# Kernel tuning notes

Measured on AMD Instinct MI355X. Metric: run time of the kernel, lower is better.

The kernel has to match this reference:

```python
import jax, jax.numpy as jnp
import numpy as np

D = 2048  # filter_dim
B = 4096  # tokens per TTT step


def setup_inputs() -> dict:
    key = jax.random.key(0)
    ks = jax.random.split(key, 8)
    s = 1.0 / np.sqrt(D)  # kaiming-ish scale so activations stay O(1)
    return {
        "src": jax.random.normal(ks[0], (B, D), jnp.float32),
        "theta_k": jax.random.normal(ks[1], (D, D), jnp.float32) * s,
        "theta_q": jax.random.normal(ks[2], (D, D), jnp.float32) * s,
        "theta_v": jax.random.normal(ks[3], (D, D), jnp.float32) * s,
        "W": jax.random.normal(ks[4], (D, D), jnp.float32) * s,
        "b": jnp.zeros((D,), jnp.float32),
        "lr_w": jax.random.uniform(ks[5], (D, D), jnp.float32) * 0.1,
        "lr_b": jax.random.uniform(ks[6], (D,), jnp.float32) * 0.1,
    }


def reference(src, theta_k, theta_q, theta_v, W, b, lr_w, lr_b):
    # Projections: src is [B, D], thetas are [D, D]
    train_view = src @ theta_k           # [B, D]
    label_view = src @ theta_v           # [B, D]
    test_view = src @ theta_q            # [B, D]

    target = label_view - train_view     # reconstruction target
    pred = train_view @ W.T + b          # nn.Linear(train_view)
    err = pred - target                  # [B, D]

    # Analytic grads of MSELoss (mean over B*D elements) wrt W ([D,D]) and b ([D])
    n = err.size  # B * D (static)
    coef = 2.0 / n
    gW = coef * (err.T @ train_view)     # [D, D], matches w.weight layout
    gb = coef * jnp.sum(err, axis=0)     # [D]

    # Per-element learning-rate SGD step (the in-place parameter rewrite)
    W_new = W - lr_w * gW
    b_new = b - lr_b * gb

    # Query with updated weights + residual
    z = test_view @ W_new.T + b_new + test_view
    return z
```

## Files before the change

kernel.cpp:

```cpp
#include <hip/hip_runtime.h>
#include <hip/hip_bf16.h>
#include <hip/hip_fp8.h>
#include <stdint.h>

#define D_DIM 2048
#define B_TOK 4096
#define COEF (2.0f / 8388608.0f)

typedef __bf16 bf16x8 __attribute__((ext_vector_type(8)));
typedef float  f32x4  __attribute__((ext_vector_type(4)));
typedef int    i32x8  __attribute__((ext_vector_type(8)));

__device__ __forceinline__ unsigned short f2bf(float f) {
  return __builtin_bit_cast(unsigned short, (__bf16)f);
}
__device__ __forceinline__ float bf2f(unsigned short u) {
  return (float)__builtin_bit_cast(__bf16, u);
}
__device__ __forceinline__ unsigned char f2f8(float f) {
  __hip_fp8_e4m3 v(f);
  return v.__x;
}

__device__ __forceinline__ void async16(const void* g, void* l) {
  __builtin_amdgcn_global_load_lds(
      (__attribute__((address_space(1))) void*)(g),
      (__attribute__((address_space(3))) void*)(l),
      16, 0, 0);
}

__device__ __forceinline__ void gemm_core_256(const unsigned short* __restrict__ Ablk,
                                              const unsigned short* __restrict__ Bblk,
                                              const int lda, const int ldb, const int KC,
                                              unsigned short* As, unsigned short* Bs,
                                              f32x4 acc[4][4]) {
  const int tid  = threadIdx.x;
  const int lane = tid & 63;
  const int wv   = tid >> 6;
  const int wm   = wv >> 1;
  const int wn   = wv & 1;
  const int t    = lane & 15;
  const int quad = lane >> 4;
  const int lrow = lane >> 3;
  const int kq   = lane & 7;
  const int kqs  = kq ^ lrow;

  const int nk = KC >> 6;

  auto stageA2 = [&](int buf, int kt, int l0) {
    const int k0 = kt << 6;
    unsigned short* Ad = As + buf * 16384;
#pragma unroll
    for (int l = l0; l < l0 + 2; ++l) {
      const int seg = wv * 4 + l;
      const int r   = seg * 8 + lrow;
      async16(Ablk + (size_t)r * lda + k0 + kqs * 8, Ad + seg * 512);
    }
  };
  auto stageB1 = [&](int buf, int kt, int l) {
    const int k0 = kt << 6;
    unsigned short* Bd = Bs + buf * 8192;
    const int seg = wv * 2 + l;
    const int r   = seg * 8 + lrow;
    async16(Bblk + (size_t)r * ldb + k0 + kqs * 8, Bd + seg * 512);
  };

  stageA2(0, 0, 0); stageA2(0, 0, 2); stageB1(0, 0, 0); stageB1(0, 0, 1);
  if (nk > 1) { stageA2(1, 1, 0); stageA2(1, 1, 2); stageB1(1, 1, 0); stageB1(1, 1, 1); }
  if (nk > 1) asm volatile("s_waitcnt vmcnt(6)" ::: "memory");
  else        asm volatile("s_waitcnt vmcnt(0)" ::: "memory");
  __builtin_amdgcn_s_barrier();

  int cur = 0;
  for (int kt = 0; kt < nk; ++kt) {
    const unsigned short* Ac = As + cur * 16384;
    const unsigned short* Bc = Bs + cur * 8192;
    const int nb = (cur >= 1) ? cur - 1 : 2;
    const bool pf = (kt + 2 < nk);

    bf16x8 af[4], bfr[4];
#pragma unroll
    for (int i = 0; i < 4; ++i) {
      const int rm = wm * 64 + i * 16 + t;
      af[i]  = *(const bf16x8*)(Ac + rm * 64 + ((quad) ^ (rm & 7)) * 8);
      const int rn = wn * 64 + i * 16 + t;
      bfr[i] = *(const bf16x8*)(Bc + rn * 64 + ((quad) ^ (rn & 7)) * 8);
    }
    __builtin_amdgcn_sched_barrier(0);
    if (pf) { stageA2(nb, kt + 2, 0); stageB1(nb, kt + 2, 0); }
    __builtin_amdgcn_sched_barrier(0);
    __builtin_amdgcn_s_barrier();
    asm volatile("s_waitcnt lgkmcnt(0)" ::: "memory");
    __builtin_amdgcn_sched_barrier(0);
    __builtin_amdgcn_s_setprio(1);
#pragma unroll
    for (int i = 0; i < 4; ++i)
#pragma unroll
      for (int j = 0; j < 4; ++j)
        acc[i][j] = __builtin_amdgcn_mfma_f32_16x16x32_bf16(af[i], bfr[j], acc[i][j], 0, 0, 0);
    __builtin_amdgcn_s_setprio(0);
    __builtin_amdgcn_sched_barrier(0);
    __builtin_amdgcn_s_barrier();

#pragma unroll
    for (int i = 0; i < 4; ++i) {
      const int rm = wm * 64 + i * 16 + t;
      af[i]  = *(const bf16x8*)(Ac + rm * 64 + ((4 + quad) ^ (rm & 7)) * 8);
      const int rn = wn * 64 + i * 16 + t;
      bfr[i] = *(const bf16x8*)(Bc + rn * 64 + ((4 + quad) ^ (rn & 7)) * 8);
    }
    __builtin_amdgcn_sched_barrier(0);
    if (pf) { stageA2(nb, kt + 2, 2); stageB1(nb, kt + 2, 1); }
    __builtin_amdgcn_sched_barrier(0);
    if (pf)               asm volatile("s_waitcnt vmcnt(6)" ::: "memory");
    else if (kt + 1 < nk) asm volatile("s_waitcnt vmcnt(0)" ::: "memory");
    __builtin_amdgcn_s_barrier();
    asm volatile("s_waitcnt lgkmcnt(0)" ::: "memory");
    __builtin_amdgcn_sched_barrier(0);
    __builtin_amdgcn_s_setprio(1);
#pragma unroll
    for (int i = 0; i < 4; ++i)
#pragma unroll
      for (int j = 0; j < 4; ++j)
        acc[i][j] = __builtin_amdgcn_mfma_f32_16x16x32_bf16(af[i], bfr[j], acc[i][j], 0, 0, 0);
    __builtin_amdgcn_s_setprio(0);
    __builtin_amdgcn_sched_barrier(0);
    __builtin_amdgcn_s_barrier();

    cur = (cur == 2) ? 0 : cur + 1;
  }
}

#define GEMM_PROLOGUE256(AP, BP, LDAv, LDBv, KCv)                              \
  __shared__ __align__(16) unsigned short As[3 * 16384];                       \
  __shared__ __align__(16) unsigned short Bs[3 * 8192];                        \
  const int lin = blockIdx.y * 16 + blockIdx.x;                                \
  const int swz = (lin & 7) * 32 + (lin >> 3);                                 \
  const int bx = swz & 15, by = swz >> 4;                                      \
  const unsigned short* Ablk = (AP) + (size_t)by * 256 * (LDAv);               \
  const unsigned short* Bblk = (BP) + (size_t)bx * 128 * (LDBv);               \
  f32x4 acc[4][4];                                                             \
  _Pragma("unroll") for (int i = 0; i < 4; ++i)                                \
  _Pragma("unroll") for (int j = 0; j < 4; ++j)                                \
      acc[i][j] = (f32x4){0.f, 0.f, 0.f, 0.f};                                 \
  gemm_core_256(Ablk, Bblk, (LDAv), (LDBv), (KCv), As, Bs, acc);               \
  const int lane = threadIdx.x & 63;                                           \
  const int wv = threadIdx.x >> 6;                                             \
  const int wm = wv >> 1, wn = wv & 1;                                         \
  const int t = lane & 15, quad = lane >> 4;                                   \
  const int gm_base = by * 256 + wm * 64;                                      \
  const int gn_base = bx * 128 + wn * 64;

__device__ __forceinline__ void gemm_core_f8(const unsigned char* __restrict__ Ablk,
                                             const unsigned char* __restrict__ Bblk,
                                             const int lda, const int ldb, const int KC,
                                             unsigned char* As, unsigned char* Bs,
                                             f32x4 acc[4][4]) {
  const int tid  = threadIdx.x;
  const int lane = tid & 63;
  const int wv   = tid >> 6;
  const int wm   = wv & 1, wn = wv >> 1;
  const int t    = lane & 15;
  const int quad = lane >> 4;
  const int lrow = lane >> 3;
  const int kq   = lane & 7;
  const int kqs  = kq ^ lrow;

  const int nk = KC >> 7;
  for (int kt = 0; kt < nk; ++kt) {
    const int k0 = kt << 7;
#pragma unroll
    for (int l = 0; l < 4; ++l) {
      const int seg = wv * 4 + l;
      const int r   = seg * 8 + lrow;
      async16(Ablk + (size_t)r * lda + k0 + kqs * 16, As + seg * 1024);
      async16(Bblk + (size_t)r * ldb + k0 + kqs * 16, Bs + seg * 1024);
    }
    __syncthreads();
    i32x8 af[4];
#pragma unroll
    for (int i = 0; i < 4; ++i) {
      const int rm = wm * 64 + i * 16 + t;
      const unsigned char* base = As + rm * 128;
      const int x = rm & 7;
      const uint4 lo = *(const uint4*)(base + (((quad << 1)    ) ^ x) * 16);
      const uint4 hi = *(const uint4*)(base + (((quad << 1) | 1) ^ x) * 16);
      af[i] = (i32x8){(int)lo.x, (int)lo.y, (int)lo.z, (int)lo.w,
                      (int)hi.x, (int)hi.y, (int)hi.z, (int)hi.w};
    }
#pragma unroll
    for (int j = 0; j < 4; ++j) {
      const int rn = wn * 64 + j * 16 + t;
      const unsigned char* base = Bs + rn * 128;
      const int x = rn & 7;
      const uint4 lo = *(const uint4*)(base + (((quad << 1)    ) ^ x) * 16);
      const uint4 hi = *(const uint4*)(base + (((quad << 1) | 1) ^ x) * 16);
      const i32x8 bq = (i32x8){(int)lo.x, (int)lo.y, (int)lo.z, (int)lo.w,
                               (int)hi.x, (int)hi.y, (int)hi.z, (int)hi.w};
#pragma unroll
      for (int i = 0; i < 4; ++i)
        acc[i][j] = __builtin_amdgcn_mfma_scale_f32_16x16x128_f8f6f4(
            af[i], bq, acc[i][j], 0, 0, 0, 127, 0, 127);
    }
    __syncthreads();
  }
}

#define GEMM8_PROLOGUE(AP, BP, LDAv, LDBv, KCv)                                \
  __shared__ __align__(16) unsigned char As8[128 * 128];                       \
  __shared__ __align__(16) unsigned char Bs8[128 * 128];                       \
  const unsigned char* Ablk = (AP) + (size_t)blockIdx.y * 128 * (LDAv);        \
  const unsigned char* Bblk = (BP) + (size_t)blockIdx.x * 128 * (LDBv);        \
  f32x4 acc[4][4];                                                             \
  _Pragma("unroll") for (int i = 0; i < 4; ++i)                                \
  _Pragma("unroll") for (int j = 0; j < 4; ++j)                                \
      acc[i][j] = (f32x4){0.f, 0.f, 0.f, 0.f};                                 \
  gemm_core_f8(Ablk, Bblk, (LDAv), (LDBv), (KCv), As8, Bs8, acc);              \
  const int lane = threadIdx.x & 63;                                           \
  const int wv = threadIdx.x >> 6;                                             \
  const int wm = wv & 1, wn = wv >> 1;                                         \
  const int t = lane & 15, quad = lane >> 4;                                   \
  const int gm_base = blockIdx.y * 128 + wm * 64;                              \
  const int gn_base = blockIdx.x * 128 + wn * 64;

__global__ __launch_bounds__(256) void gemm_train_f8(
    const unsigned char* __restrict__ srcA,
    const unsigned char* __restrict__ thkT8,
    unsigned char* __restrict__ src_cat_f8,
    unsigned char* __restrict__ trainT8) {
  GEMM8_PROLOGUE(srcA, thkT8, 4096, 2048, 2048)
  unsigned char* scr = ((wv >> 1) ? Bs8 : As8) + (wv & 1) * 2304;
#pragma unroll
  for (int p = 0; p < 2; ++p) {
#pragma unroll
    for (int jl = 0; jl < 2; ++jl) {
      const int j = p * 2 + jl;
      const int gn = gn_base + j * 16 + t;
#pragma unroll
      for (int i = 0; i < 4; ++i) {
        const int gm0 = gm_base + i * 16 + quad * 4;
        uchar4 pk = make_uchar4(f2f8(acc[i][j][0]), f2f8(acc[i][j][1]),
                                f2f8(acc[i][j][2]), f2f8(acc[i][j][3]));
        src_cat_f8[(size_t)(gm0 + 0) * 4096 + gn] = pk.x;
        src_cat_f8[(size_t)(gm0 + 1) * 4096 + gn] = pk.y;
        src_cat_f8[(size_t)(gm0 + 2) * 4096 + gn] = pk.z;
        src_cat_f8[(size_t)(gm0 + 3) * 4096 + gn] = pk.w;
        *(uchar4*)(scr + (jl * 16 + t) * 72 + i * 16 + quad * 4) = pk;
      }
    }
    __syncthreads();
    const int row = lane >> 3, chunk = lane & 7;
#pragma unroll
    for (int q = 0; q < 4; ++q) {
      const int rr = q * 8 + row;
      const uint2 v = *(const uint2*)(scr + rr * 72 + chunk * 8);
      *(uint2*)(trainT8 + (size_t)(gn_base + p * 32 + rr) * B_TOK + gm_base + chunk * 8) = v;
    }
    __syncthreads();
  }
}

__global__ __launch_bounds__(512, 2) void gemm_test(
    const unsigned short* __restrict__ src_bf,
    const unsigned short* __restrict__ thqT,
    unsigned short* __restrict__ testv) {
  GEMM_PROLOGUE256(src_bf, thqT, 2048, 2048, 2048)
#pragma unroll
  for (int i = 0; i < 4; ++i) {
#pragma unroll
    for (int j = 0; j < 4; ++j) {
      const int gm0 = gm_base + i * 16 + quad * 4;
      const int gn  = gn_base + j * 16 + t;
#pragma unroll
      for (int r = 0; r < 4; ++r)
        testv[(size_t)(gm0 + r) * D_DIM + gn] = f2bf(acc[i][j][r]);
    }
  }
}

__global__ __launch_bounds__(256) void gemm_err_f8(
    const unsigned char* __restrict__ src_cat_f8,
    const unsigned char* __restrict__ Wcat_f8,
    const float* __restrict__ bvec,
    unsigned char* __restrict__ errT8,
    float* __restrict__ gb) {
  GEMM8_PROLOGUE(src_cat_f8, Wcat_f8, 4096, 4096, 4096)
  unsigned char* scr = ((wv >> 1) ? Bs8 : As8) + (wv & 1) * 2304;
#pragma unroll
  for (int p = 0; p < 2; ++p) {
#pragma unroll
    for (int jl = 0; jl < 2; ++jl) {
      const int j = p * 2 + jl;
      const int gn = gn_base + j * 16 + t;
      const float bias = bvec[gn];
      float cs = 0.f;
#pragma unroll
      for (int i = 0; i < 4; ++i) {
        const float e0 = acc[i][j][0] + bias, e1 = acc[i][j][1] + bias;
        const float e2 = acc[i][j][2] + bias, e3 = acc[i][j][3] + bias;
        *(uchar4*)(scr + (jl * 16 + t) * 72 + i * 16 + quad * 4) =
            make_uchar4(f2f8(e0), f2f8(e1), f2f8(e2), f2f8(e3));
        cs += e0 + e1 + e2 + e3;
      }
      cs += __shfl_xor(cs, 16);
      cs += __shfl_xor(cs, 32);
      if (quad == 0) atomicAdd(&gb[gn], cs);
    }
    __syncthreads();
    const int row = lane >> 3, chunk = lane & 7;
#pragma unroll
    for (int q = 0; q < 4; ++q) {
      const int rr = q * 8 + row;
      const uint2 v = *(const uint2*)(scr + rr * 72 + chunk * 8);
      *(uint2*)(errT8 + (size_t)(gn_base + p * 32 + rr) * B_TOK + gm_base + chunk * 8) = v;
    }
    __syncthreads();
  }
}

__global__ __launch_bounds__(256) void gemm_gw_f8(
    const unsigned char* __restrict__ errT8,
    const unsigned char* __restrict__ trainT8,
    float* __restrict__ P0, float* __restrict__ P1) {
  const int z = blockIdx.z;
  const unsigned char* Abase = errT8 + z * 2048;
  const unsigned char* Bbase = trainT8 + z * 2048;
  GEMM8_PROLOGUE(Abase, Bbase, B_TOK, B_TOK, 2048)
  float* P = (z == 0) ? P0 : P1;
#pragma unroll
  for (int i = 0; i < 4; ++i) {
#pragma unroll
    for (int j = 0; j < 4; ++j) {
      const int gm0 = gm_base + i * 16 + quad * 4;
      const int gn  = gn_base + j * 16 + t;
#pragma unroll
      for (int r = 0; r < 4; ++r)
        P[(size_t)(gm0 + r) * D_DIM + gn] = acc[i][j][r];
    }
  }
}

__global__ __launch_bounds__(256) void wnew_reduce(
    const float* __restrict__ P0, const float* __restrict__ P1,
    const float* __restrict__ W, const float* __restrict__ lr_w,
    unsigned short* __restrict__ Wnew) {
  const int i = blockIdx.x * 256 + threadIdx.x;
  const float4 p0 = ((const float4*)P0)[i];
  const float4 p1 = ((const float4*)P1)[i];
  const float4 w  = ((const float4*)W)[i];
  const float4 l  = ((const float4*)lr_w)[i];
  ((ushort4*)Wnew)[i] = make_ushort4(
      f2bf(w.x - l.x * (COEF * (p0.x + p1.x))),
      f2bf(w.y - l.y * (COEF * (p0.y + p1.y))),
      f2bf(w.z - l.z * (COEF * (p0.z + p1.z))),
      f2bf(w.w - l.w * (COEF * (p0.w + p1.w))));
}

__global__ __launch_bounds__(512, 2) void gemm_out(
    const unsigned short* __restrict__ testv,
    const unsigned short* __restrict__ Wnew,
    const float* __restrict__ bvec,
    const float* __restrict__ lr_b,
    const float* __restrict__ gb,
    float* __restrict__ out) {
  GEMM_PROLOGUE256(testv, Wnew, 2048, 2048, 2048)
#pragma unroll
  for (int j = 0; j < 4; ++j) {
    const int gn = gn_base + j * 16 + t;
    const float bias = bvec[gn] - lr_b[gn] * (COEF * gb[gn]);
#pragma unroll
    for (int i = 0; i < 4; ++i) {
      const int gm0 = gm_base + i * 16 + quad * 4;
#pragma unroll
      for (int r = 0; r < 4; ++r) {
        const size_t idx = (size_t)(gm0 + r) * D_DIM + gn;
        out[idx] = acc[i][j][r] + bias + bf2f(testv[idx]);
      }
    }
  }
}

__global__ __launch_bounds__(256) void cvt_all(const float* __restrict__ src,
                                               const float* __restrict__ W,
                                               unsigned short* __restrict__ src_bf,
                                               unsigned char* __restrict__ src_cat_f8,
                                               unsigned char* __restrict__ Wcat_f8,
                                               float* __restrict__ gb) {
  const int i = blockIdx.x * 256 + threadIdx.x;
  if (i < 512) ((float4*)gb)[i] = (float4){0.f, 0.f, 0.f, 0.f};
  if (i < 2097152) {
    const int m = i >> 9, c = i & 511;
    const float4 v = ((const float4*)src)[i];
    ((ushort4*)src_bf)[i] = make_ushort4(f2bf(v.x), f2bf(v.y), f2bf(v.z), f2bf(v.w));
    *(uchar4*)(src_cat_f8 + (size_t)m * 4096 + 2048 + c * 4) =
        make_uchar4(f2f8(v.x), f2f8(v.y), f2f8(v.z), f2f8(v.w));
  } else {
    const int j = i - 2097152;
    const int n = j >> 9, c = j & 511;
    const float4 v = ((const float4*)W)[j];
    *(uchar4*)(Wcat_f8 + (size_t)n * 4096 + c * 4) =
        make_uchar4(f2f8(v.x), f2f8(v.y), f2f8(v.z), f2f8(v.w));
  }
}

__global__ __launch_bounds__(256) void tcvt(
    const float* __restrict__ thk, const float* __restrict__ thq,
    const float* __restrict__ thv,
    unsigned char* __restrict__ thkT8, unsigned short* __restrict__ thqT,
    unsigned char* __restrict__ Wcat_f8) {
  __shared__ float tile[32][33];
  const int z = blockIdx.z;
  const int bx = blockIdx.x * 32, by = blockIdx.y * 32;
  const int tx = threadIdx.x & 31, ty = threadIdx.x >> 5;
#pragma unroll
  for (int l = 0; l < 4; ++l) {
    const int r = ty + l * 8;
    const size_t idx = (size_t)(by + r) * D_DIM + bx + tx;
    tile[r][tx] = (z == 0) ? thk[idx] : (z == 1) ? thq[idx] : (thk[idx] - thv[idx]);
  }
  __syncthreads();
#pragma unroll
  for (int l = 0; l < 4; ++l) {
    const int r = ty + l * 8;
    if (z == 0)
      thkT8[(size_t)(bx + r) * 2048 + by + tx] = f2f8(tile[tx][r]);
    else if (z == 1)
      thqT[(size_t)(bx + r) * 2048 + by + tx] = f2bf(tile[tx][r]);
    else
      Wcat_f8[(size_t)(bx + r) * 4096 + 2048 + by + tx] = f2f8(tile[tx][r]);
  }
}

extern "C" void kernel_launch(void* const* d_in, const int* in_sizes, int n_in,
                              void* d_out, int out_size, void* d_ws, size_t ws_size,
                              hipStream_t stream) {
  const float* src = (const float*)d_in[0];
  const float* thk = (const float*)d_in[1];
  const float* thq = (const float*)d_in[2];
  const float* thv = (const float*)d_in[3];
  const float* W   = (const float*)d_in[4];
  const float* bv  = (const float*)d_in[5];
  const float* lrw = (const float*)d_in[6];
  const float* lrb = (const float*)d_in[7];
  float* out = (float*)d_out;

  char* ws = (char*)d_ws;
  const size_t MB = 1024 * 1024;
  unsigned short* src_bf     = (unsigned short*)(ws + 0);
  unsigned char*  src_cat_f8 = (unsigned char*)(ws + 16 * MB);
  unsigned char*  Wcat_f8    = (unsigned char*)(ws + 32 * MB);
  unsigned char*  thkT8      = (unsigned char*)(ws + 40 * MB);
  unsigned short* thqT       = (unsigned short*)(ws + 44 * MB);
  unsigned char*  trainT8    = (unsigned char*)(ws + 52 * MB);
  unsigned short* testv      = (unsigned short*)(ws + 60 * MB);
  unsigned char*  errT8      = (unsigned char*)(ws + 76 * MB);
  unsigned short* WnewBf     = (unsigned short*)(ws + 84 * MB);
  float*          P0         = (float*)(ws + 92 * MB);
  float*          P1         = (float*)(ws + 108 * MB);
  float*          gb         = (float*)(ws + 124 * MB);

  cvt_all<<<12288, 256, 0, stream>>>(src, W, src_bf, src_cat_f8, Wcat_f8, gb);
  tcvt<<<dim3(64, 64, 3), 256, 0, stream>>>(thk, thq, thv, thkT8, thqT, Wcat_f8);

  gemm_train_f8<<<dim3(16, 32), 256, 0, stream>>>(src_cat_f8 + 2048, thkT8,
                                                  src_cat_f8, trainT8);
  gemm_test<<<dim3(16, 16), 512, 0, stream>>>(src_bf, thqT, testv);
  gemm_err_f8<<<dim3(16, 32), 256, 0, stream>>>(src_cat_f8, Wcat_f8, bv, errT8, gb);
  gemm_gw_f8<<<dim3(16, 16, 2), 256, 0, stream>>>(errT8, trainT8, P0, P1);
  wnew_reduce<<<4096, 256, 0, stream>>>(P0, P1, W, lrw, WnewBf);
  gemm_out<<<dim3(16, 16), 512, 0, stream>>>(testv, WnewBf, bv, lrb, gb, out);
}
```

Before: 341.0 us.

## Triple-buffer FP8 GEMM core with 256x128 tiles and block swizzle

Replaces the single-buffered 128x128 FP8 MFMA core with a 256x128-tile, 512-thread core. Global-to-LDS copies for tile kt+2 are issued while MFMAs run on tile kt, across three LDS buffers. Each K step is split into two MFMA halves with explicit waitcnt, barriers and setprio. Block indices are swizzled for L2 locality, and the train, err and gW grids are halved to match. The goal is to hide load latency and raise reuse per tile, at the cost of 144KB of LDS per block, which limits occupancy to one block per CU.

Result: no change. 335.7 us (-1.6%).

```diff
diff --git a/kernel.cpp b/kernel.cpp
--- a/kernel.cpp
+++ b/kernel.cpp
@@ -151,15 +151,16 @@
   const int gm_base = by * 256 + wm * 64;                                      \
   const int gn_base = bx * 128 + wn * 64;
 
-__device__ __forceinline__ void gemm_core_f8(const unsigned char* __restrict__ Ablk,
-                                             const unsigned char* __restrict__ Bblk,
-                                             const int lda, const int ldb, const int KC,
-                                             unsigned char* As, unsigned char* Bs,
-                                             f32x4 acc[4][4]) {
+__device__ __forceinline__ void gemm_core_f8_256(const unsigned char* __restrict__ Ablk,
+                                                 const unsigned char* __restrict__ Bblk,
+                                                 const int lda, const int ldb, const int KC,
+                                                 unsigned char* As, unsigned char* Bs,
+                                                 f32x4 acc[4][4]) {
   const int tid  = threadIdx.x;
   const int lane = tid & 63;
   const int wv   = tid >> 6;
-  const int wm   = wv & 1, wn = wv >> 1;
+  const int wm   = wv >> 1;
+  const int wn   = wv & 1;
   const int t    = lane & 15;
   const int quad = lane >> 4;
   const int lrow = lane >> 3;
@@ -167,69 +168,133 @@
   const int kqs  = kq ^ lrow;
 
   const int nk = KC >> 7;
-  for (int kt = 0; kt < nk; ++kt) {
+
+  auto stageA2 = [&](int buf, int kt, int l0) {
     const int k0 = kt << 7;
-#pragma unroll
-    for (int l = 0; l < 4; ++l) {
+    unsigned char* Ad = As + buf * 32768;
+#pragma unroll
+    for (int l = l0; l < l0 + 2; ++l) {
       const int seg = wv * 4 + l;
       const int r   = seg * 8 + lrow;
-      async16(Ablk + (size_t)r * lda + k0 + kqs * 16, As + seg * 1024);
-      async16(Bblk + (size_t)r * ldb + k0 + kqs * 16, Bs + seg * 1024);
-    }
-    __syncthreads();
-    i32x8 af[4];
+      async16(Ablk + (size_t)r * lda + k0 + kqs * 16, Ad + seg * 1024);
+    }
+  };
+  auto stageB1 = [&](int buf, int kt, int l) {
+    const int k0 = kt << 7;
+    unsigned char* Bd = Bs + buf * 16384;
+    const int seg = wv * 2 + l;
+    const int r   = seg * 8 + lrow;
+    async16(Bblk + (size_t)r * ldb + k0 + kqs * 16, Bd + seg * 1024);
+  };
+
+  auto readF = [&](const unsigned char* base, int x) -> i32x8 {
+    const uint4 lo = *(const uint4*)(base + (((quad << 1)    ) ^ x) * 16);
+    const uint4 hi = *(const uint4*)(base + (((quad << 1) | 1) ^ x) * 16);
+    return (i32x8){(int)lo.x, (int)lo.y, (int)lo.z, (int)lo.w,
+                   (int)hi.x, (int)hi.y, (int)hi.z, (int)hi.w};
+  };
+
+  stageA2(0, 0, 0); stageA2(0, 0, 2); stageB1(0, 0, 0); stageB1(0, 0, 1);
+  if (nk > 1) { stageA2(1, 1, 0); stageA2(1, 1, 2); stageB1(1, 1, 0); stageB1(1, 1, 1); }
+  if (nk > 1) asm volatile("s_waitcnt vmcnt(6)" ::: "memory");
+  else        asm volatile("s_waitcnt vmcnt(0)" ::: "memory");
+  __builtin_amdgcn_s_barrier();
+
+  int cur = 0;
+  for (int kt = 0; kt < nk; ++kt) {
+    const unsigned char* Ac = As + cur * 32768;
+    const unsigned char* Bc = Bs + cur * 16384;
+    const int nb = (cur >= 1) ? cur - 1 : 2;
+    const bool pf = (kt + 2 < nk);
+
+    i32x8 af[4], bq0, bq1;
 #pragma unroll
     for (int i = 0; i < 4; ++i) {
       const int rm = wm * 64 + i * 16 + t;
-      const unsigned char* base = As + rm * 128;
-      const int x = rm & 7;
-      const uint4 lo = *(const uint4*)(base + (((quad << 1)    ) ^ x) * 16);
-      const uint4 hi = *(const uint4*)(base + (((quad << 1) | 1) ^ x) * 16);
-      af[i] = (i32x8){(int)lo.x, (int)lo.y, (int)lo.z, (int)lo.w,
-                      (int)hi.x, (int)hi.y, (int)hi.z, (int)hi.w};
-    }
-#pragma unroll
-    for (int j = 0; j < 4; ++j) {
-      const int rn = wn * 64 + j * 16 + t;
-      const unsigned char* base = Bs + rn * 128;
-      const int x = rn & 7;
-      const uint4 lo = *(const uint4*)(base + (((quad << 1)    ) ^ x) * 16);
-      const uint4 hi = *(const uint4*)(base + (((quad << 1) | 1) ^ x) * 16);
-      const i32x8 bq = (i32x8){(int)lo.x, (int)lo.y, (int)lo.z, (int)lo.w,
-                               (int)hi.x, (int)hi.y, (int)hi.z, (int)hi.w};
-#pragma unroll
-      for (int i = 0; i < 4; ++i)
-        acc[i][j] = __builtin_amdgcn_mfma_scale_f32_16x16x128_f8f6f4(
-            af[i], bq, acc[i][j], 0, 0, 0, 127, 0, 127);
-    }
-    __syncthreads();
-  }
-}
-
-#define GEMM8_PROLOGUE(AP, BP, LDAv, LDBv, KCv)                                \
-  __shared__ __align__(16) unsigned char As8[128 * 128];                       \
-  __shared__ __align__(16) unsigned char Bs8[128 * 128];                       \
-  const unsigned char* Ablk = (AP) + (size_t)blockIdx.y * 128 * (LDAv);        \
-  const unsigned char* Bblk = (BP) + (size_t)blockIdx.x * 128 * (LDBv);        \
+      af[i] = readF(Ac + rm * 128, rm & 7);
+    }
+    {
+      const int rn0 = wn * 64 + 0 * 16 + t;
+      bq0 = readF(Bc + rn0 * 128, rn0 & 7);
+      const int rn1 = wn * 64 + 1 * 16 + t;
+      bq1 = readF(Bc + rn1 * 128, rn1 & 7);
+    }
+    __builtin_amdgcn_sched_barrier(0);
+    if (pf) { stageA2(nb, kt + 2, 0); stageB1(nb, kt + 2, 0); }
+    __builtin_amdgcn_sched_barrier(0);
+    __builtin_amdgcn_s_barrier();
+    asm volatile("s_waitcnt lgkmcnt(0)" ::: "memory");
+    __builtin_amdgcn_sched_barrier(0);
+    __builtin_amdgcn_s_setprio(1);
+#pragma unroll
+    for (int i = 0; i < 4; ++i) {
+      acc[i][0] = __builtin_amdgcn_mfma_scale_f32_16x16x128_f8f6f4(
+          af[i], bq0, acc[i][0], 0, 0, 0, 127, 0, 127);
+      acc[i][1] = __builtin_amdgcn_mfma_scale_f32_16x16x128_f8f6f4(
+          af[i], bq1, acc[i][1], 0, 0, 0, 127, 0, 127);
+    }
+    __builtin_amdgcn_s_setprio(0);
+    __builtin_amdgcn_sched_barrier(0);
+    __builtin_amdgcn_s_barrier();
+
+    {
+      const int rn2 = wn * 64 + 2 * 16 + t;
+      bq0 = readF(Bc + rn2 * 128, rn2 & 7);
+      const int rn3 = wn * 64 + 3 * 16 + t;
+      bq1 = readF(Bc + rn3 * 128, rn3 & 7);
+    }
+    __builtin_amdgcn_sched_barrier(0);
+    if (pf) { stageA2(nb, kt + 2, 2); stageB1(nb, kt + 2, 1); }
+    __builtin_amdgcn_sched_barrier(0);
+    if (pf)               asm volatile("s_waitcnt vmcnt(6)" ::: "memory");
+    else if (kt + 1 < nk) asm volatile("s_waitcnt vmcnt(0)" ::: "memory");
+    __builtin_amdgcn_s_barrier();
+    asm volatile("s_waitcnt lgkmcnt(0)" ::: "memory");
+    __builtin_amdgcn_sched_barrier(0);
+    __builtin_amdgcn_s_setprio(1);
+#pragma unroll
+    for (int i = 0; i < 4; ++i) {
+      acc[i][2] = __builtin_amdgcn_mfma_scale_f32_16x16x128_f8f6f4(
+          af[i], bq0, acc[i][2], 0, 0, 0, 127, 0, 127);
+      acc[i][3] = __builtin_amdgcn_mfma_scale_f32_16x16x128_f8f6f4(
+          af[i], bq1, acc[i][3], 0, 0, 0, 127, 0, 127);
+    }
+    __builtin_amdgcn_s_setprio(0);
+    __builtin_amdgcn_sched_barrier(0);
+    __builtin_amdgcn_s_barrier();
+
+    cur = (cur == 2) ? 0 : cur + 1;
+  }
+}
+
+#define GEMM8_PROLOGUE256(AP, BP, LDAv, LDBv, KCv)                             \
+  __shared__ __align__(16) unsigned char As8[3 * 32768];                       \
+  __shared__ __align__(16) unsigned char Bs8[3 * 16384];                       \
+  const int nwg = gridDim.x * gridDim.y;                                       \
+  const int lin = blockIdx.y * 16 + blockIdx.x;                                \
+  const int swz = (lin & 7) * (nwg >> 3) + (lin >> 3);                         \
+  const int bx = swz & 15, by = swz >> 4;                                      \
+  const unsigned char* Ablk = (AP) + (size_t)by * 256 * (LDAv);                \
+  const unsigned char* Bblk = (BP) + (size_t)bx * 128 * (LDBv);                \
   f32x4 acc[4][4];                                                             \
   _Pragma("unroll") for (int i = 0; i < 4; ++i)                                \
   _Pragma("unroll") for (int j = 0; j < 4; ++j)                                \
       acc[i][j] = (f32x4){0.f, 0.f, 0.f, 0.f};                                 \
-  gemm_core_f8(Ablk, Bblk, (LDAv), (LDBv), (KCv), As8, Bs8, acc);              \
+  gemm_core_f8_256(Ablk, Bblk, (LDAv), (LDBv), (KCv), As8, Bs8, acc);          \
   const int lane = threadIdx.x & 63;                                           \
   const int wv = threadIdx.x >> 6;                                             \
-  const int wm = wv & 1, wn = wv >> 1;                                         \
+  const int wm = wv >> 1, wn = wv & 1;                                         \
   const int t = lane & 15, quad = lane >> 4;                                   \
-  const int gm_base = blockIdx.y * 128 + wm * 64;                              \
-  const int gn_base = blockIdx.x * 128 + wn * 64;
-
-__global__ __launch_bounds__(256) void gemm_train_f8(
+  const int gm_base = by * 256 + wm * 64;                                      \
+  const int gn_base = bx * 128 + wn * 64;
+
+__global__ __launch_bounds__(512, 2) void gemm_train_f8(
     const unsigned char* __restrict__ srcA,
     const unsigned char* __restrict__ thkT8,
     unsigned char* __restrict__ src_cat_f8,
     unsigned char* __restrict__ trainT8) {
-  GEMM8_PROLOGUE(srcA, thkT8, 4096, 2048, 2048)
-  unsigned char* scr = ((wv >> 1) ? Bs8 : As8) + (wv & 1) * 2304;
+  GEMM8_PROLOGUE256(srcA, thkT8, 4096, 2048, 2048)
+  unsigned char* scr = As8 + wv * 2304;
 #pragma unroll
   for (int p = 0; p < 2; ++p) {
 #pragma unroll
@@ -278,14 +343,14 @@
   }
 }
 
-__global__ __launch_bounds__(256) void gemm_err_f8(
+__global__ __launch_bounds__(512, 2) void gemm_err_f8(
     const unsigned char* __restrict__ src_cat_f8,
     const unsigned char* __restrict__ Wcat_f8,
     const float* __restrict__ bvec,
     unsigned char* __restrict__ errT8,
     float* __restrict__ gb) {
-  GEMM8_PROLOGUE(src_cat_f8, Wcat_f8, 4096, 4096, 4096)
-  unsigned char* scr = ((wv >> 1) ? Bs8 : As8) + (wv & 1) * 2304;
+  GEMM8_PROLOGUE256(src_cat_f8, Wcat_f8, 4096, 4096, 4096)
+  unsigned char* scr = As8 + wv * 2304;
 #pragma unroll
   for (int p = 0; p < 2; ++p) {
 #pragma unroll
@@ -318,14 +383,14 @@
   }
 }
 
-__global__ __launch_bounds__(256) void gemm_gw_f8(
+__global__ __launch_bounds__(512, 2) void gemm_gw_f8(
     const unsigned char* __restrict__ errT8,
     const unsigned char* __restrict__ trainT8,
     float* __restrict__ P0, float* __restrict__ P1) {
   const int z = blockIdx.z;
   const unsigned char* Abase = errT8 + z * 2048;
   const unsigned char* Bbase = trainT8 + z * 2048;
-  GEMM8_PROLOGUE(Abase, Bbase, B_TOK, B_TOK, 2048)
+  GEMM8_PROLOGUE256(Abase, Bbase, B_TOK, B_TOK, 2048)
   float* P = (z == 0) ? P0 : P1;
 #pragma unroll
   for (int i = 0; i < 4; ++i) {
@@ -462,11 +527,11 @@
   cvt_all<<<12288, 256, 0, stream>>>(src, W, src_bf, src_cat_f8, Wcat_f8, gb);
   tcvt<<<dim3(64, 64, 3), 256, 0, stream>>>(thk, thq, thv, thkT8, thqT, Wcat_f8);
 
-  gemm_train_f8<<<dim3(16, 32), 256, 0, stream>>>(src_cat_f8 + 2048, thkT8,
+  gemm_train_f8<<<dim3(16, 16), 512, 0, stream>>>(src_cat_f8 + 2048, thkT8,
                                                   src_cat_f8, trainT8);
   gemm_test<<<dim3(16, 16), 512, 0, stream>>>(src_bf, thqT, testv);
-  gemm_err_f8<<<dim3(16, 32), 256, 0, stream>>>(src_cat_f8, Wcat_f8, bv, errT8, gb);
-  gemm_gw_f8<<<dim3(16, 16, 2), 256, 0, stream>>>(errT8, trainT8, P0, P1);
+  gemm_err_f8<<<dim3(16, 16), 512, 0, stream>>>(src_cat_f8, Wcat_f8, bv, errT8, gb);
+  gemm_gw_f8<<<dim3(16, 8, 2), 512, 0, stream>>>(errT8, trainT8, P0, P1);
   wnew_reduce<<<4096, 256, 0, stream>>>(P0, P1, W, lrw, WnewBf);
   gemm_out<<<dim3(16, 16), 512, 0, stream>>>(testv, WnewBf, bv, lrb, gb, out);
 }
```
